# Optimization experiments

Measured on AMD Instinct MI355X. Metric: run time of the kernel, lower is better.

## Reference

```python
import jax, jax.numpy as jnp
import numpy as np

N = 50000   # nodes
E = 800000  # directed edges (avg degree 16)
IN, HID, OUT = 128, 128, 64


def setup_inputs() -> dict:
    key = jax.random.key(0)
    k1, k2, k3, k4 = jax.random.split(key, 4)
    x = jax.random.normal(k1, (N, IN), dtype=jnp.float32)
    edge_index = jax.random.randint(k2, (2, E), 0, N, dtype=jnp.int64)
    W1 = jax.random.normal(k3, (IN, HID), dtype=jnp.float32) * (1.0 / np.sqrt(IN))
    b1 = jnp.zeros((HID,), dtype=jnp.float32)
    W2 = jax.random.normal(k4, (HID, OUT), dtype=jnp.float32) * (1.0 / np.sqrt(HID))
    b2 = jnp.zeros((OUT,), dtype=jnp.float32)
    return {"x": x, "edge_index": edge_index, "W1": W1, "b1": b1, "W2": W2, "b2": b2}


def _gcn_conv(x, src, dst, deg_inv_sqrt, W, b):
    # PyG GCNConv: h = X @ W; out_i = sum_j norm_ij * h_j  (edges incl. self-loops); out += b
    h = x @ W                                   # [N, F_out]
    norm = deg_inv_sqrt[src] * deg_inv_sqrt[dst]  # [E+N]
    msg = h[src] * norm[:, None]                # gather + scale
    out = jax.ops.segment_sum(msg, dst, num_segments=x.shape[0])  # scatter-add
    return out + b


def reference(x, edge_index, W1, b1, W2, b2):
    n = x.shape[0]
    loop = jnp.arange(n, dtype=edge_index.dtype)
    # add self-loops once; shared by both layers
    src = jnp.concatenate([edge_index[0], loop])
    dst = jnp.concatenate([edge_index[1], loop])
    deg = jax.ops.segment_sum(jnp.ones_like(src, dtype=x.dtype), dst, num_segments=n)
    deg_inv_sqrt = jnp.where(deg > 0, jax.lax.rsqrt(jnp.maximum(deg, 1.0)), 0.0)

    h = _gcn_conv(x, src, dst, deg_inv_sqrt, W1, b1)
    h = jax.nn.relu(h)
    out = _gcn_conv(h, src, dst, deg_inv_sqrt, W2, b2)
    return out
```

## Files before the change

kernel.cpp:

```cpp
#include <hip/hip_runtime.h>

typedef unsigned short u16;
typedef unsigned int u32;
typedef __attribute__((ext_vector_type(8))) short bf16x8;
typedef __attribute__((ext_vector_type(4))) float f32x4;

#define IN_F 128
#define CAP  8192
#define EPB  8192

__device__ inline float bf2f(u16 v) {
    return __uint_as_float(((unsigned)v) << 16);
}
__device__ inline u16 f2bf(float f) {
    unsigned u = __float_as_uint(f);
    return (u16)((u + 0x7fffu + ((u >> 16) & 1u)) >> 16);
}

__device__ inline int block_scan_excl(int v, int* sdat) {
    int tid = threadIdx.x;
    sdat[tid] = v;
    __syncthreads();
#pragma unroll
    for (int off = 1; off < 256; off <<= 1) {
        int t = (tid >= off) ? sdat[tid - off] : 0;
        __syncthreads();
        sdat[tid] += t;
        __syncthreads();
    }
    return sdat[tid] - v;
}


template<int M>
__device__ inline void packW_body(const float* __restrict__ W, u16* __restrict__ Wp, int t) {
    constexpr int NCT = M / 16;
    int l  = t & 63;
    int q  = t >> 6;
    int kt = q & 3;
    int q2 = q >> 2;
    int ct = q2 % NCT;
    int h  = q2 / NCT;
    int col   = 16 * ct + (l & 15);
    int krow0 = 32 * kt + 8 * (l >> 4);
    u16* outp = Wp + (size_t)t * 8;
#pragma unroll
    for (int r = 0; r < 8; ++r) {
        float w  = W[(size_t)(krow0 + r) * M + col];
        u16 hi   = f2bf(w);
        outp[r] = (h == 0) ? hi : f2bf(w - bf2f(hi));
    }
}

__global__ __launch_bounds__(256) void k_setup(const float* __restrict__ W1,
                                               const float* __restrict__ W2,
                                               u16* __restrict__ w1p,
                                               u16* __restrict__ w2p,
                                               int* bcur, int nbuk) {
    int t = blockIdx.x * 256 + threadIdx.x;
    if (t < nbuk) bcur[t] = 0;
    if (t < 2 * 8 * 4 * 64) packW_body<128>(W1, w1p, t);
    if (t < 2 * 4 * 4 * 64) packW_body<64>(W2, w2p, t);
}


__global__ __launch_bounds__(256) void k_ag1(const float* __restrict__ X,
                                             const u16* __restrict__ Wp,
                                             u16* __restrict__ Y,
                                             const int* __restrict__ ei,
                                             int* bcur, u32* __restrict__ tmp,
                                             int E, int n, int nbuk, int gb) {
    constexpr int NCT = 8;
    constexpr int WPW = 2 * NCT * 4 * 64 * 8;
    __shared__ u16 wlds[WPW];
    __shared__ int hist[256];
    const int tid = threadIdx.x;

    if (blockIdx.x < gb) {
        for (int i = tid; i < WPW / 8; i += 256)
            ((uint4*)wlds)[i] = ((const uint4*)Wp)[i];
        __syncthreads();
        const int wid = tid >> 6;
        const int l   = tid & 63;
        const int lr  = l & 15;
        const int lg  = l >> 4;
#pragma unroll
        for (int rt = 0; rt < 4; ++rt) {
            const int row0 = blockIdx.x * 256 + rt * 64 + wid * 16;
            const int arow = row0 + lr;
            const bool rowok = arow < n;
            const float* xr = X + (size_t)arow * 128;
            bf16x8 ahi[4], alo[4];
#pragma unroll
            for (int kt = 0; kt < 4; ++kt) {
                float v[8];
                if (rowok) {
                    float4 p0 = *(const float4*)(xr + 32 * kt + 8 * lg);
                    float4 p1 = *(const float4*)(xr + 32 * kt + 8 * lg + 4);
                    v[0] = p0.x; v[1] = p0.y; v[2] = p0.z; v[3] = p0.w;
                    v[4] = p1.x; v[5] = p1.y; v[6] = p1.z; v[7] = p1.w;
                } else {
#pragma unroll
                    for (int r = 0; r < 8; ++r) v[r] = 0.f;
                }
#pragma unroll
                for (int r = 0; r < 8; ++r) {
                    u16 hi = f2bf(v[r]);
                    ahi[kt][r] = (short)hi;
                    alo[kt][r] = (short)f2bf(v[r] - bf2f(hi));
                }
            }
#pragma unroll
            for (int ct = 0; ct < NCT; ++ct) {
                f32x4 acc = {0.f, 0.f, 0.f, 0.f};
                const u16* whi = wlds + (size_t)(ct * 4) * 512 + l * 8;
                const u16* wlo = whi + (size_t)NCT * 4 * 512;
#pragma unroll
                for (int kt = 0; kt < 4; ++kt) {
                    bf16x8 bh = *(const bf16x8*)(whi + kt * 512);
                    bf16x8 bl = *(const bf16x8*)(wlo + kt * 512);
                    acc = __builtin_amdgcn_mfma_f32_16x16x32_bf16(ahi[kt], bh, acc, 0, 0, 0);
                    acc = __builtin_amdgcn_mfma_f32_16x16x32_bf16(alo[kt], bh, acc, 0, 0, 0);
                    acc = __builtin_amdgcn_mfma_f32_16x16x32_bf16(ahi[kt], bl, acc, 0, 0, 0);
                }
#pragma unroll
                for (int r = 0; r < 4; ++r) {
                    int row = row0 + lg * 4 + r;
                    if (row < n) Y[(size_t)row * 128 + 16 * ct + lr] = f2bf(acc[r]);
                }
            }
        }
    } else {
        const int b = blockIdx.x - gb;
        const int EN = E + n;
        const int t0 = b * EPB;
        const int t1 = min(t0 + EPB, EN);
        hist[tid] = 0;
        __syncthreads();
        for (int t = t0 + tid * 4; t < t1; t += 1024) {
            if (t + 4 <= t1 && t + 4 <= E) {
                int4 d4 = *(const int4*)(ei + E + t);
                atomicAdd(&hist[d4.x >> 8], 1);
                atomicAdd(&hist[d4.y >> 8], 1);
                atomicAdd(&hist[d4.z >> 8], 1);
                atomicAdd(&hist[d4.w >> 8], 1);
            } else {
#pragma unroll
                for (int j = 0; j < 4; ++j) {
                    int tt = t + j;
                    if (tt >= t1) break;
                    int d = (tt < E) ? ei[E + tt] : (tt - E);
                    atomicAdd(&hist[d >> 8], 1);
                }
            }
        }
        __syncthreads();
        if (tid < nbuk) {
            int r = hist[tid];
            int g = (r > 0) ? atomicAdd(&bcur[tid], r) : 0;
            hist[tid] = tid * CAP + g;
        }
        __syncthreads();
        for (int t = t0 + tid * 4; t < t1; t += 1024) {
            if (t + 4 <= t1 && t + 4 <= E) {
                int4 s4 = *(const int4*)(ei + t);
                int4 d4 = *(const int4*)(ei + E + t);
                int p0 = atomicAdd(&hist[d4.x >> 8], 1);
                int p1 = atomicAdd(&hist[d4.y >> 8], 1);
                int p2 = atomicAdd(&hist[d4.z >> 8], 1);
                int p3 = atomicAdd(&hist[d4.w >> 8], 1);
                if (p0 < ((d4.x >> 8) + 1) * CAP) tmp[p0] = (u32)s4.x | ((u32)(d4.x & 255) << 16);
                if (p1 < ((d4.y >> 8) + 1) * CAP) tmp[p1] = (u32)s4.y | ((u32)(d4.y & 255) << 16);
                if (p2 < ((d4.z >> 8) + 1) * CAP) tmp[p2] = (u32)s4.z | ((u32)(d4.z & 255) << 16);
                if (p3 < ((d4.w >> 8) + 1) * CAP) tmp[p3] = (u32)s4.w | ((u32)(d4.w & 255) << 16);
            } else {
#pragma unroll
                for (int j = 0; j < 4; ++j) {
                    int tt = t + j;
                    if (tt >= t1) break;
                    int s, d;
                    if (tt < E) { s = ei[tt]; d = ei[E + tt]; }
                    else        { s = tt - E; d = s; }
                    int bk = d >> 8;
                    int pos = atomicAdd(&hist[bk], 1);
                    if (pos < (bk + 1) * CAP)
                        tmp[pos] = (u32)s | ((u32)(d & 255) << 16);
                }
            }
        }
    }
}

__global__ __launch_bounds__(256) void k_binB1(const u32* __restrict__ tmp,
                                               const int* __restrict__ bcur,
                                               int* __restrict__ row_ptr,
                                               float* __restrict__ dis,
                                               int n, int nbuk) {
    __shared__ int sdat[256];
    __shared__ int cnt_l[256];
    __shared__ int s_gbase;
    const int b = blockIdx.x;
    const int tid = threadIdx.x;
    int v = (tid < nbuk) ? min(bcur[tid], CAP) : 0;
    int ex0 = block_scan_excl(v, sdat);
    if (tid == b) s_gbase = ex0;
    if (b == nbuk - 1 && tid == 0) row_ptr[n] = sdat[255];
    __syncthreads();
    const int gbase = s_gbase;
    const int total = min(bcur[b], CAP);
    const u32* rec0 = tmp + (size_t)b * CAP;
    cnt_l[tid] = 0;
    __syncthreads();
    for (int i = tid; i < total; i += 256)
        atomicAdd(&cnt_l[rec0[i] >> 16], 1);
    __syncthreads();
    int deg = cnt_l[tid];
    int ex = block_scan_excl(deg, sdat);
    int node = b * 256 + tid;
    if (node < n) {
        row_ptr[node] = gbase + ex;
        dis[node] = rsqrtf((float)deg);
    }
}

__global__ __launch_bounds__(256) void k_binB2(const u32* __restrict__ tmp,
                                               const int* __restrict__ bcur,
                                               const int* __restrict__ row_ptr,
                                               const float* __restrict__ dis,
                                               u32* __restrict__ es, int n) {
    __shared__ int lcur[256];
    __shared__ float ldis[256];
    __shared__ u32 es_lds[CAP];
    const int b = blockIdx.x;
    const int tid = threadIdx.x;
    const int total = min(bcur[b], CAP);
    const int node0 = b * 256;
    const int gbase = row_ptr[node0];
    int node = node0 + tid;
    lcur[tid] = (node < n) ? (row_ptr[node] - gbase) : 0;
    ldis[tid] = (node < n) ? dis[node] : 0.f;
    __syncthreads();
    const u32* rec0 = tmp + (size_t)b * CAP;
    for (int i = tid; i < total; i += 256) {
        u32 rec = rec0[i];
        int dl = rec >> 16;
        int s  = rec & 0xffff;
        float nrm = dis[s] * ldis[dl];
        int p = atomicAdd(&lcur[dl], 1);
        es_lds[p] = (u32)s | ((u32)f2bf(nrm) << 16);
    }
    __syncthreads();
    for (int i = tid; i < total; i += 256)
        es[gbase + i] = es_lds[i];
}


__global__ __launch_bounds__(256) void k_gemm2(const u16* __restrict__ A,
                                               const u16* __restrict__ Wp,
                                               u16* __restrict__ Y, int n) {
    constexpr int NCT = 4;
    constexpr int WPW = 2 * NCT * 4 * 64 * 8;
    __shared__ u16 wlds[WPW];
    for (int i = threadIdx.x; i < WPW / 8; i += 256)
        ((uint4*)wlds)[i] = ((const uint4*)Wp)[i];
    __syncthreads();
    const int wid = threadIdx.x >> 6;
    const int l   = threadIdx.x & 63;
    const int lr  = l & 15;
    const int lg  = l >> 4;
#pragma unroll
    for (int rt = 0; rt < 4; ++rt) {
        const int row0 = blockIdx.x * 256 + rt * 64 + wid * 16;
        const int arow = row0 + lr;
        const bool rowok = arow < n;
        bf16x8 a[4];
#pragma unroll
        for (int kt = 0; kt < 4; ++kt) {
            if (rowok) {
                a[kt] = *(const bf16x8*)(A + (size_t)arow * 128 + 32 * kt + 8 * lg);
            } else {
#pragma unroll
                for (int r = 0; r < 8; ++r) a[kt][r] = 0;
            }
        }
#pragma unroll
        for (int ct = 0; ct < NCT; ++ct) {
            f32x4 acc = {0.f, 0.f, 0.f, 0.f};
            const u16* whi = wlds + (size_t)(ct * 4) * 512 + l * 8;
            const u16* wlo = whi + (size_t)NCT * 4 * 512;
#pragma unroll
            for (int kt = 0; kt < 4; ++kt) {
                bf16x8 bh = *(const bf16x8*)(whi + kt * 512);
                bf16x8 bl = *(const bf16x8*)(wlo + kt * 512);
                acc = __builtin_amdgcn_mfma_f32_16x16x32_bf16(a[kt], bh, acc, 0, 0, 0);
                acc = __builtin_amdgcn_mfma_f32_16x16x32_bf16(a[kt], bl, acc, 0, 0, 0);
            }
#pragma unroll
            for (int r = 0; r < 4; ++r) {
                int row = row0 + lg * 4 + r;
                if (row < n) Y[(size_t)row * 64 + 16 * ct + lr] = f2bf(acc[r]);
            }
        }
    }
}


__global__ __launch_bounds__(256) void k_agg128(const u16* __restrict__ h,
                                                const int* __restrict__ row_ptr,
                                                const u32* __restrict__ es,
                                                const float* __restrict__ bias,
                                                u16* __restrict__ out, int n) {
    int node = blockIdx.x * 4 + (threadIdx.x >> 6);
    if (node >= n) return;
    int lane = threadIdx.x & 63;
    int half = lane >> 5;
    int li   = lane & 31;
    int beg = row_ptr[node], end = row_ptr[node + 1];
    const u16* hp = h + li * 4;
    float a0 = 0.f, a1 = 0.f, a2 = 0.f, a3 = 0.f;
    float b0 = 0.f, b1 = 0.f, b2 = 0.f, b3 = 0.f;
    float c0 = 0.f, c1 = 0.f, c2 = 0.f, c3 = 0.f;
    float d0 = 0.f, d1 = 0.f, d2 = 0.f, d3 = 0.f;
    int e = beg + half;
    for (; e + 14 < end; e += 16) {
        u32 r0 = es[e],      r1 = es[e + 2],  r2 = es[e + 4],  r3 = es[e + 6];
        u32 r4 = es[e + 8],  r5 = es[e + 10], r6 = es[e + 12], r7 = es[e + 14];
        ushort4 v0 = *(const ushort4*)(hp + (size_t)(r0 & 0xffff) * 128);
        ushort4 v1 = *(const ushort4*)(hp + (size_t)(r1 & 0xffff) * 128);
        ushort4 v2 = *(const ushort4*)(hp + (size_t)(r2 & 0xffff) * 128);
        ushort4 v3 = *(const ushort4*)(hp + (size_t)(r3 & 0xffff) * 128);
        ushort4 v4 = *(const ushort4*)(hp + (size_t)(r4 & 0xffff) * 128);
        ushort4 v5 = *(const ushort4*)(hp + (size_t)(r5 & 0xffff) * 128);
        ushort4 v6 = *(const ushort4*)(hp + (size_t)(r6 & 0xffff) * 128);
        ushort4 v7 = *(const ushort4*)(hp + (size_t)(r7 & 0xffff) * 128);
        float w0 = bf2f((u16)(r0 >> 16)), w1 = bf2f((u16)(r1 >> 16));
        float w2 = bf2f((u16)(r2 >> 16)), w3 = bf2f((u16)(r3 >> 16));
        float w4 = bf2f((u16)(r4 >> 16)), w5 = bf2f((u16)(r5 >> 16));
        float w6 = bf2f((u16)(r6 >> 16)), w7 = bf2f((u16)(r7 >> 16));
        a0 += w0 * bf2f(v0.x); a1 += w0 * bf2f(v0.y);
        a2 += w0 * bf2f(v0.z); a3 += w0 * bf2f(v0.w);
        b0 += w1 * bf2f(v1.x); b1 += w1 * bf2f(v1.y);
        b2 += w1 * bf2f(v1.z); b3 += w1 * bf2f(v1.w);
        c0 += w2 * bf2f(v2.x); c1 += w2 * bf2f(v2.y);
        c2 += w2 * bf2f(v2.z); c3 += w2 * bf2f(v2.w);
        d0 += w3 * bf2f(v3.x); d1 += w3 * bf2f(v3.y);
        d2 += w3 * bf2f(v3.z); d3 += w3 * bf2f(v3.w);
        a0 += w4 * bf2f(v4.x); a1 += w4 * bf2f(v4.y);
        a2 += w4 * bf2f(v4.z); a3 += w4 * bf2f(v4.w);
        b0 += w5 * bf2f(v5.x); b1 += w5 * bf2f(v5.y);
        b2 += w5 * bf2f(v5.z); b3 += w5 * bf2f(v5.w);
        c0 += w6 * bf2f(v6.x); c1 += w6 * bf2f(v6.y);
        c2 += w6 * bf2f(v6.z); c3 += w6 * bf2f(v6.w);
        d0 += w7 * bf2f(v7.x); d1 += w7 * bf2f(v7.y);
        d2 += w7 * bf2f(v7.z); d3 += w7 * bf2f(v7.w);
    }
    for (; e < end; e += 2) {
        u32 r0 = es[e];
        float w0 = bf2f((u16)(r0 >> 16));
        ushort4 v0 = *(const ushort4*)(hp + (size_t)(r0 & 0xffff) * 128);
        a0 += w0 * bf2f(v0.x); a1 += w0 * bf2f(v0.y);
        a2 += w0 * bf2f(v0.z); a3 += w0 * bf2f(v0.w);
    }
    a0 = (a0 + b0) + (c0 + d0);
    a1 = (a1 + b1) + (c1 + d1);
    a2 = (a2 + b2) + (c2 + d2);
    a3 = (a3 + b3) + (c3 + d3);
    a0 += __shfl_xor(a0, 32, 64);
    a1 += __shfl_xor(a1, 32, 64);
    a2 += __shfl_xor(a2, 32, 64);
    a3 += __shfl_xor(a3, 32, 64);
    if (half == 0) {
        float4 bv = *(const float4*)(bias + 4 * li);
        a0 = fmaxf(a0 + bv.x, 0.f);
        a1 = fmaxf(a1 + bv.y, 0.f);
        a2 = fmaxf(a2 + bv.z, 0.f);
        a3 = fmaxf(a3 + bv.w, 0.f);
        ushort4 o;
        o.x = f2bf(a0); o.y = f2bf(a1); o.z = f2bf(a2); o.w = f2bf(a3);
        *(ushort4*)(out + (size_t)node * 128 + 4 * li) = o;
    }
}


__global__ __launch_bounds__(256) void k_agg64(const u16* __restrict__ h,
                                               const int* __restrict__ row_ptr,
                                               const u32* __restrict__ es,
                                               const float* __restrict__ bias,
                                               float* __restrict__ out, int n) {
    int node = blockIdx.x * 4 + (threadIdx.x >> 6);
    if (node >= n) return;
    int lane = threadIdx.x & 63;
    int q  = lane >> 4;
    int li = lane & 15;
    int beg = row_ptr[node], end = row_ptr[node + 1];
    const u16* hp = h + li * 4;
    float a0 = 0.f, a1 = 0.f, a2 = 0.f, a3 = 0.f;
    float b0 = 0.f, b1 = 0.f, b2 = 0.f, b3 = 0.f;
    float c0 = 0.f, c1 = 0.f, c2 = 0.f, c3 = 0.f;
    float d0 = 0.f, d1 = 0.f, d2 = 0.f, d3 = 0.f;
    int e = beg + q;
    for (; e + 12 < end; e += 16) {
        u32 r0 = es[e], r1 = es[e + 4], r2 = es[e + 8], r3 = es[e + 12];
        ushort4 v0 = *(const ushort4*)(hp + (size_t)(r0 & 0xffff) * 64);
        ushort4 v1 = *(const ushort4*)(hp + (size_t)(r1 & 0xffff) * 64);
        ushort4 v2 = *(const ushort4*)(hp + (size_t)(r2 & 0xffff) * 64);
        ushort4 v3 = *(const ushort4*)(hp + (size_t)(r3 & 0xffff) * 64);
        float w0 = bf2f((u16)(r0 >> 16)), w1 = bf2f((u16)(r1 >> 16));
        float w2 = bf2f((u16)(r2 >> 16)), w3 = bf2f((u16)(r3 >> 16));
        a0 += w0 * bf2f(v0.x); a1 += w0 * bf2f(v0.y);
        a2 += w0 * bf2f(v0.z); a3 += w0 * bf2f(v0.w);
        b0 += w1 * bf2f(v1.x); b1 += w1 * bf2f(v1.y);
        b2 += w1 * bf2f(v1.z); b3 += w1 * bf2f(v1.w);
        c0 += w2 * bf2f(v2.x); c1 += w2 * bf2f(v2.y);
        c2 += w2 * bf2f(v2.z); c3 += w2 * bf2f(v2.w);
        d0 += w3 * bf2f(v3.x); d1 += w3 * bf2f(v3.y);
        d2 += w3 * bf2f(v3.z); d3 += w3 * bf2f(v3.w);
    }
    for (; e < end; e += 4) {
        u32 r0 = es[e];
        float w0 = bf2f((u16)(r0 >> 16));
        ushort4 v0 = *(const ushort4*)(hp + (size_t)(r0 & 0xffff) * 64);
        a0 += w0 * bf2f(v0.x); a1 += w0 * bf2f(v0.y);
        a2 += w0 * bf2f(v0.z); a3 += w0 * bf2f(v0.w);
    }
    a0 = (a0 + b0) + (c0 + d0);
    a1 = (a1 + b1) + (c1 + d1);
    a2 = (a2 + b2) + (c2 + d2);
    a3 = (a3 + b3) + (c3 + d3);
    a0 += __shfl_xor(a0, 16, 64); a0 += __shfl_xor(a0, 32, 64);
    a1 += __shfl_xor(a1, 16, 64); a1 += __shfl_xor(a1, 32, 64);
    a2 += __shfl_xor(a2, 16, 64); a2 += __shfl_xor(a2, 32, 64);
    a3 += __shfl_xor(a3, 16, 64); a3 += __shfl_xor(a3, 32, 64);
    if (q == 0) {
        float4 bv = *(const float4*)(bias + 4 * li);
        float4 o;
        o.x = a0 + bv.x; o.y = a1 + bv.y; o.z = a2 + bv.z; o.w = a3 + bv.w;
        *(float4*)(out + (size_t)node * 64 + 4 * li) = o;
    }
}


static inline char* alignp(char* p, size_t a) {
    return (char*)(((uintptr_t)p + a - 1) & ~(uintptr_t)(a - 1));
}

extern "C" void kernel_launch(void* const* d_in, const int* in_sizes, int n_in,
                              void* d_out, int out_size, void* d_ws, size_t ws_size,
                              hipStream_t stream) {
    const float* x  = (const float*)d_in[0];
    const int*   ei = (const int*)d_in[1];
    const float* W1 = (const float*)d_in[2];
    const float* b1 = (const float*)d_in[3];
    const float* W2 = (const float*)d_in[4];
    const float* b2 = (const float*)d_in[5];
    float* out = (float*)d_out;

    const int n     = in_sizes[0] / IN_F;
    const int E     = in_sizes[1] / 2;
    const int EN    = E + n;
    const int NBUK  = (n + 255) / 256;
    const int GB    = (n + 255) / 256;
    const int NBLKA = (EN + EPB - 1) / EPB;

    char* w = (char*)d_ws;
    int*   row_ptr  = (int*)w;   w = alignp(w + (size_t)(n + 1) * 4, 256);
    int*   bcur     = (int*)w;   w = alignp(w + (size_t)NBUK * 4, 256);
    float* dis      = (float*)w; w = alignp(w + (size_t)n * 4, 256);
    u32*   tmp      = (u32*)w;   w = alignp(w + (size_t)NBUK * CAP * 4, 256);
    u32*   es       = (u32*)w;   w = alignp(w + (size_t)EN * 4, 256);
    u16*   w1p      = (u16*)w;   w = alignp(w + (size_t)2 * 8 * 4 * 64 * 8 * 2, 256);
    u16*   w2p      = (u16*)w;   w = alignp(w + (size_t)2 * 4 * 4 * 64 * 8 * 2, 256);
    u16*   h1b      = (u16*)w;   w = alignp(w + (size_t)n * 128 * 2, 256);
    u16*   a1b      = (u16*)w;   w = alignp(w + (size_t)n * 128 * 2, 256);
    u16*   h2b      = h1b;

    k_setup<<<16, 256, 0, stream>>>(W1, W2, w1p, w2p, bcur, NBUK);
    k_ag1<<<GB + NBLKA, 256, 0, stream>>>(x, w1p, h1b, ei, bcur, tmp, E, n, NBUK, GB);
    k_binB1<<<NBUK, 256, 0, stream>>>(tmp, bcur, row_ptr, dis, n, NBUK);
    k_binB2<<<NBUK, 256, 0, stream>>>(tmp, bcur, row_ptr, dis, es, n);

    k_agg128<<<(n + 3) / 4, 256, 0, stream>>>(h1b, row_ptr, es, b1, a1b, n);
    k_gemm2<<<GB, 256, 0, stream>>>(a1b, w2p, h2b, n);
    k_agg64<<<(n + 3) / 4, 256, 0, stream>>>(h2b, row_ptr, es, b2, out, n);
}
```

Baseline: 126.6 us.

## Assign one sub-wave group per node in aggregation kernels, drop cross-lane reductions

The aggregation kernels now map 32 lanes (layer 1) or 16 lanes (layer 2) to each destination node instead of a whole 64-lane wave, so each wave handles 2 or 4 nodes and the edge loop walks edges sequentially with 4-way unroll. This removes the shuffle reductions and idle lanes at output time, and packs more nodes per block. In exchange each lane group has less memory-level parallelism per node (4 outstanding gathers instead of 8 or 16 across the wave), and nodes sharing a wave diverge in degree. EPB is also reduced, which changes the edge-binning block granularity.

Result: faster. 117.4 us, median of 2 (-7.2%).

```diff
diff --git a/kernel.cpp b/kernel.cpp
--- a/kernel.cpp
+++ b/kernel.cpp
@@ -7,7 +7,7 @@
 
 #define IN_F 128
 #define CAP  8192
-#define EPB  8192
+#define EPB  2048
 
 __device__ inline float bf2f(u16 v) {
     return __uint_as_float(((unsigned)v) << 16);
@@ -310,33 +310,24 @@
                                                 const u32* __restrict__ es,
                                                 const float* __restrict__ bias,
                                                 u16* __restrict__ out, int n) {
-    int node = blockIdx.x * 4 + (threadIdx.x >> 6);
+    int node = blockIdx.x * 8 + (threadIdx.x >> 5);
     if (node >= n) return;
-    int lane = threadIdx.x & 63;
-    int half = lane >> 5;
-    int li   = lane & 31;
+    int l31 = threadIdx.x & 31;
     int beg = row_ptr[node], end = row_ptr[node + 1];
-    const u16* hp = h + li * 4;
+    const u16* hp = h + l31 * 4;
     float a0 = 0.f, a1 = 0.f, a2 = 0.f, a3 = 0.f;
     float b0 = 0.f, b1 = 0.f, b2 = 0.f, b3 = 0.f;
     float c0 = 0.f, c1 = 0.f, c2 = 0.f, c3 = 0.f;
     float d0 = 0.f, d1 = 0.f, d2 = 0.f, d3 = 0.f;
-    int e = beg + half;
-    for (; e + 14 < end; e += 16) {
-        u32 r0 = es[e],      r1 = es[e + 2],  r2 = es[e + 4],  r3 = es[e + 6];
-        u32 r4 = es[e + 8],  r5 = es[e + 10], r6 = es[e + 12], r7 = es[e + 14];
+    int e = beg;
+    for (; e + 3 < end; e += 4) {
+        u32 r0 = es[e], r1 = es[e + 1], r2 = es[e + 2], r3 = es[e + 3];
         ushort4 v0 = *(const ushort4*)(hp + (size_t)(r0 & 0xffff) * 128);
         ushort4 v1 = *(const ushort4*)(hp + (size_t)(r1 & 0xffff) * 128);
         ushort4 v2 = *(const ushort4*)(hp + (size_t)(r2 & 0xffff) * 128);
         ushort4 v3 = *(const ushort4*)(hp + (size_t)(r3 & 0xffff) * 128);
-        ushort4 v4 = *(const ushort4*)(hp + (size_t)(r4 & 0xffff) * 128);
-        ushort4 v5 = *(const ushort4*)(hp + (size_t)(r5 & 0xffff) * 128);
-        ushort4 v6 = *(const ushort4*)(hp + (size_t)(r6 & 0xffff) * 128);
-        ushort4 v7 = *(const ushort4*)(hp + (size_t)(r7 & 0xffff) * 128);
         float w0 = bf2f((u16)(r0 >> 16)), w1 = bf2f((u16)(r1 >> 16));
         float w2 = bf2f((u16)(r2 >> 16)), w3 = bf2f((u16)(r3 >> 16));
-        float w4 = bf2f((u16)(r4 >> 16)), w5 = bf2f((u16)(r5 >> 16));
-        float w6 = bf2f((u16)(r6 >> 16)), w7 = bf2f((u16)(r7 >> 16));
         a0 += w0 * bf2f(v0.x); a1 += w0 * bf2f(v0.y);
         a2 += w0 * bf2f(v0.z); a3 += w0 * bf2f(v0.w);
         b0 += w1 * bf2f(v1.x); b1 += w1 * bf2f(v1.y);
@@ -345,16 +336,8 @@
         c2 += w2 * bf2f(v2.z); c3 += w2 * bf2f(v2.w);
         d0 += w3 * bf2f(v3.x); d1 += w3 * bf2f(v3.y);
         d2 += w3 * bf2f(v3.z); d3 += w3 * bf2f(v3.w);
-        a0 += w4 * bf2f(v4.x); a1 += w4 * bf2f(v4.y);
-        a2 += w4 * bf2f(v4.z); a3 += w4 * bf2f(v4.w);
-        b0 += w5 * bf2f(v5.x); b1 += w5 * bf2f(v5.y);
-        b2 += w5 * bf2f(v5.z); b3 += w5 * bf2f(v5.w);
-        c0 += w6 * bf2f(v6.x); c1 += w6 * bf2f(v6.y);
-        c2 += w6 * bf2f(v6.z); c3 += w6 * bf2f(v6.w);
-        d0 += w7 * bf2f(v7.x); d1 += w7 * bf2f(v7.y);
-        d2 += w7 * bf2f(v7.z); d3 += w7 * bf2f(v7.w);
-    }
-    for (; e < end; e += 2) {
+    }
+    for (; e < end; ++e) {
         u32 r0 = es[e];
         float w0 = bf2f((u16)(r0 >> 16));
         ushort4 v0 = *(const ushort4*)(hp + (size_t)(r0 & 0xffff) * 128);
@@ -365,20 +348,14 @@
     a1 = (a1 + b1) + (c1 + d1);
     a2 = (a2 + b2) + (c2 + d2);
     a3 = (a3 + b3) + (c3 + d3);
-    a0 += __shfl_xor(a0, 32, 64);
-    a1 += __shfl_xor(a1, 32, 64);
-    a2 += __shfl_xor(a2, 32, 64);
-    a3 += __shfl_xor(a3, 32, 64);
-    if (half == 0) {
-        float4 bv = *(const float4*)(bias + 4 * li);
-        a0 = fmaxf(a0 + bv.x, 0.f);
-        a1 = fmaxf(a1 + bv.y, 0.f);
-        a2 = fmaxf(a2 + bv.z, 0.f);
-        a3 = fmaxf(a3 + bv.w, 0.f);
-        ushort4 o;
-        o.x = f2bf(a0); o.y = f2bf(a1); o.z = f2bf(a2); o.w = f2bf(a3);
-        *(ushort4*)(out + (size_t)node * 128 + 4 * li) = o;
-    }
+    float4 bv = *(const float4*)(bias + 4 * l31);
+    a0 = fmaxf(a0 + bv.x, 0.f);
+    a1 = fmaxf(a1 + bv.y, 0.f);
+    a2 = fmaxf(a2 + bv.z, 0.f);
+    a3 = fmaxf(a3 + bv.w, 0.f);
+    ushort4 o;
+    o.x = f2bf(a0); o.y = f2bf(a1); o.z = f2bf(a2); o.w = f2bf(a3);
+    *(ushort4*)(out + (size_t)node * 128 + 4 * l31) = o;
 }
 
 
@@ -387,20 +364,18 @@
                                                const u32* __restrict__ es,
                                                const float* __restrict__ bias,
                                                float* __restrict__ out, int n) {
-    int node = blockIdx.x * 4 + (threadIdx.x >> 6);
+    int node = blockIdx.x * 16 + (threadIdx.x >> 4);
     if (node >= n) return;
-    int lane = threadIdx.x & 63;
-    int q  = lane >> 4;
-    int li = lane & 15;
+    int l16 = threadIdx.x & 15;
     int beg = row_ptr[node], end = row_ptr[node + 1];
-    const u16* hp = h + li * 4;
+    const u16* hp = h + l16 * 4;
     float a0 = 0.f, a1 = 0.f, a2 = 0.f, a3 = 0.f;
     float b0 = 0.f, b1 = 0.f, b2 = 0.f, b3 = 0.f;
     float c0 = 0.f, c1 = 0.f, c2 = 0.f, c3 = 0.f;
     float d0 = 0.f, d1 = 0.f, d2 = 0.f, d3 = 0.f;
-    int e = beg + q;
-    for (; e + 12 < end; e += 16) {
-        u32 r0 = es[e], r1 = es[e + 4], r2 = es[e + 8], r3 = es[e + 12];
+    int e = beg;
+    for (; e + 3 < end; e += 4) {
+        u32 r0 = es[e], r1 = es[e + 1], r2 = es[e + 2], r3 = es[e + 3];
         ushort4 v0 = *(const ushort4*)(hp + (size_t)(r0 & 0xffff) * 64);
         ushort4 v1 = *(const ushort4*)(hp + (size_t)(r1 & 0xffff) * 64);
         ushort4 v2 = *(const ushort4*)(hp + (size_t)(r2 & 0xffff) * 64);
@@ -416,7 +391,7 @@
         d0 += w3 * bf2f(v3.x); d1 += w3 * bf2f(v3.y);
         d2 += w3 * bf2f(v3.z); d3 += w3 * bf2f(v3.w);
     }
-    for (; e < end; e += 4) {
+    for (; e < end; ++e) {
         u32 r0 = es[e];
         float w0 = bf2f((u16)(r0 >> 16));
         ushort4 v0 = *(const ushort4*)(hp + (size_t)(r0 & 0xffff) * 64);
@@ -427,16 +402,10 @@
     a1 = (a1 + b1) + (c1 + d1);
     a2 = (a2 + b2) + (c2 + d2);
     a3 = (a3 + b3) + (c3 + d3);
-    a0 += __shfl_xor(a0, 16, 64); a0 += __shfl_xor(a0, 32, 64);
-    a1 += __shfl_xor(a1, 16, 64); a1 += __shfl_xor(a1, 32, 64);
-    a2 += __shfl_xor(a2, 16, 64); a2 += __shfl_xor(a2, 32, 64);
-    a3 += __shfl_xor(a3, 16, 64); a3 += __shfl_xor(a3, 32, 64);
-    if (q == 0) {
-        float4 bv = *(const float4*)(bias + 4 * li);
-        float4 o;
-        o.x = a0 + bv.x; o.y = a1 + bv.y; o.z = a2 + bv.z; o.w = a3 + bv.w;
-        *(float4*)(out + (size_t)node * 64 + 4 * li) = o;
-    }
+    float4 bv = *(const float4*)(bias + 4 * l16);
+    float4 o;
+    o.x = a0 + bv.x; o.y = a1 + bv.y; o.z = a2 + bv.z; o.w = a3 + bv.w;
+    *(float4*)(out + (size_t)node * 64 + 4 * l16) = o;
 }
 
 
@@ -479,7 +448,7 @@
     k_binB1<<<NBUK, 256, 0, stream>>>(tmp, bcur, row_ptr, dis, n, NBUK);
     k_binB2<<<NBUK, 256, 0, stream>>>(tmp, bcur, row_ptr, dis, es, n);
 
-    k_agg128<<<(n + 3) / 4, 256, 0, stream>>>(h1b, row_ptr, es, b1, a1b, n);
+    k_agg128<<<(n + 7) / 8, 256, 0, stream>>>(h1b, row_ptr, es, b1, a1b, n);
     k_gemm2<<<GB, 256, 0, stream>>>(a1b, w2p, h2b, n);
-    k_agg64<<<(n + 3) / 4, 256, 0, stream>>>(h2b, row_ptr, es, b2, out, n);
-}
+    k_agg64<<<(n + 15) / 16, 256, 0, stream>>>(h2b, row_ptr, es, b2, out, n);
+}
```
